# Optimization experiments

Measured on AMD Instinct MI355X. Metric: run time of the kernel, lower is better.

Reference implementation:

```python
import jax, jax.numpy as jnp
import numpy as np

K = 3   # spatial_kernel_size
M = 5   # memory_size


def setup_inputs() -> dict:
    key = jax.random.key(0)
    ks = jax.random.split(key, 16)
    C = 64
    B, H, D, W = 2, 24, 24, 24
    s = 0.05
    n = jax.random.normal
    return {
        "x": n(ks[0], (B, C, H, D, W), jnp.float32),
        "prev_memory": jnp.zeros((B, C), jnp.float32),
        "Wq": n(ks[1], (C, C), jnp.float32) * s,
        "bq": n(ks[2], (C,), jnp.float32) * s,
        "Wk": n(ks[3], (C, C), jnp.float32) * s,
        "bk": n(ks[4], (C,), jnp.float32) * s,
        "Wv": n(ks[5], (C, C), jnp.float32) * s,
        "bv": n(ks[6], (C,), jnp.float32) * s,
        "mem_key": n(ks[7], (C, M), jnp.float32),
        "mem_value": n(ks[8], (C, M), jnp.float32),
        "Wg": n(ks[9], (C, 2 * C), jnp.float32) * s,
        "bg": n(ks[10], (C,), jnp.float32) * s,
        "W_ih": n(ks[11], (3 * C, C), jnp.float32) * s,
        "W_hh": n(ks[12], (3 * C, C), jnp.float32) * s,
        "b_ih": n(ks[13], (3 * C,), jnp.float32) * s,
        "b_hh": n(ks[14], (3 * C,), jnp.float32) * s,
    }


def _patches(x, k):
    # x: (B,C,H,D,W) -> (B,C,k^3,H,D,W) local neighborhoods (zero-padded)
    B, C, H, D, W = x.shape
    p = k // 2
    xp = jnp.pad(x, ((0, 0), (0, 0), (p, p), (p, p), (p, p)))
    sl = [xp[:, :, i:i + H, j:j + D, l:l + W]
          for i in range(k) for j in range(k) for l in range(k)]
    return jnp.stack(sl, axis=2)


def reference(x, prev_memory, Wq, bq, Wk, bk, Wv, bv, mem_key, mem_value,
              Wg, bg, W_ih, W_hh, b_ih, b_hh):
    B, C, H, D, W = x.shape
    N = H * D * W
    xf = x.reshape(B, C, N)
    pf = _patches(x, K).reshape(B, C, K ** 3, N)

    # 1x1x1 conv projections (pure channel mixes)
    q = jnp.einsum('oc,bcn->bon', Wq, xf) + bq[None, :, None]            # (B,C,N)
    k_sp = jnp.einsum('oc,bcmn->bomn', Wk, pf) + bk[None, :, None, None]  # (B,C,27,N)
    v_sp = jnp.einsum('oc,bcmn->bomn', Wv, pf) + bv[None, :, None, None]

    # memory tokens broadcast over all spatial locations
    k_mem = jnp.broadcast_to(mem_key[None, :, :, None], (B, C, M, N))
    v_mem = jnp.broadcast_to(mem_value[None, :, :, None], (B, C, M, N))
    kk = jnp.concatenate([k_mem, k_sp], axis=2)   # (B,C,M+27,N)
    vv = jnp.concatenate([v_mem, v_sp], axis=2)

    # per-channel scalar attention over memory+neighborhood axis
    attn = jax.nn.softmax(q[:, :, None, :] * kk / jnp.sqrt(jnp.float32(C)), axis=2)
    out = jnp.sum(attn * vv, axis=2).reshape(B, C, H, D, W)

    # sigmoid gate over concat([x, out])
    gin = jnp.concatenate([xf, out.reshape(B, C, N)], axis=1)  # (B,2C,N)
    gate = jax.nn.sigmoid(jnp.einsum('oc,bcn->bon', Wg, gin)
                          + bg[None, :, None]).reshape(B, C, H, D, W)
    out = gate * out + (1.0 - gate) * x

    # GRU memory update on spatially pooled features (torch GRUCell math)
    mu = out.mean(axis=(2, 3, 4))                 # (B,C)
    gi = mu @ W_ih.T + b_ih
    gh = prev_memory @ W_hh.T + b_hh
    ir, iz, ii = jnp.split(gi, 3, axis=1)
    hr, hz, hn = jnp.split(gh, 3, axis=1)
    r = jax.nn.sigmoid(ir + hr)
    z = jax.nn.sigmoid(iz + hz)
    ng = jnp.tanh(ii + r * hn)
    new_memory = (1.0 - z) * ng + z * prev_memory
    return out, new_memory
```

## Files before the change

kernel.cpp:

```cpp
#include <hip/hip_runtime.h>
#include <math.h>

#define NPOS 13824
#define CDIM 64
#define BTCH 2
#define LOG2E 1.4426950408889634f
#define QSCALE (0.125f * LOG2E)

__device__ __forceinline__ unsigned int f2bf1(float f) {
  unsigned int u = __float_as_uint(f);
  return (u + 0x7FFFu + ((u >> 16) & 1u)) >> 16;
}

__global__ __launch_bounds__(256) void qkvg_kernel(
    const float* __restrict__ x,
    const float* __restrict__ Wq, const float* __restrict__ bq,
    const float* __restrict__ Wk, const float* __restrict__ bk,
    const float* __restrict__ Wv, const float* __restrict__ bv,
    const float* __restrict__ Wg,
    float* __restrict__ Qb, float* __restrict__ Kb, float* __restrict__ Vb,
    float* __restrict__ GXb, float* __restrict__ XT, float* __restrict__ pool)
{
  __shared__ __align__(16) float wqt[64*68];
  __shared__ __align__(16) float wkt[64*68];
  __shared__ __align__(16) float wvt[64*68];
  __shared__ __align__(16) float wgt[64*68];
  const int t  = threadIdx.x;
  const int bi = blockIdx.x;
  const int b  = bi / 216;
  const int n0 = (bi - b*216) * 64;
  if (bi == 0 && t < 128) pool[t] = 0.0f;

  #pragma unroll
  for (int k = 0; k < 16; ++k) {
    int idx = t + k*256;
    int lo = idx & 63, hi = idx >> 6;
    wqt[lo*68 + hi] = Wq[idx] * QSCALE;
    wkt[lo*68 + hi] = Wk[idx];
    wvt[lo*68 + hi] = Wv[idx];
    wgt[lo*68 + hi] = Wg[hi*128 + lo];
  }
  __syncthreads();

  const int c0  = (t & 15) * 4;
  const int nn0 = (t >> 4) * 4;
  const float* xbase = x + (size_t)(b*64)*NPOS + n0 + nn0;
  float aq[4][4] = {}; float ak[4][4] = {}; float av[4][4] = {}; float ag[4][4] = {};
  #pragma unroll 4
  for (int cp = 0; cp < 64; ++cp) {
    const float4 xv4 = *(const float4*)(xbase + (size_t)cp*NPOS);
    const float4 q4  = *(const float4*)&wqt[cp*68 + c0];
    const float4 k4  = *(const float4*)&wkt[cp*68 + c0];
    const float4 v4  = *(const float4*)&wvt[cp*68 + c0];
    const float4 g4  = *(const float4*)&wgt[cp*68 + c0];
    const float xa[4] = {xv4.x, xv4.y, xv4.z, xv4.w};
    const float qa[4] = {q4.x, q4.y, q4.z, q4.w};
    const float ka[4] = {k4.x, k4.y, k4.z, k4.w};
    const float va[4] = {v4.x, v4.y, v4.z, v4.w};
    const float ga[4] = {g4.x, g4.y, g4.z, g4.w};
    #pragma unroll
    for (int ci = 0; ci < 4; ++ci)
      #pragma unroll
      for (int ni = 0; ni < 4; ++ni) {
        aq[ci][ni] = fmaf(qa[ci], xa[ni], aq[ci][ni]);
        ak[ci][ni] = fmaf(ka[ci], xa[ni], ak[ci][ni]);
        av[ci][ni] = fmaf(va[ci], xa[ni], av[ci][ni]);
        ag[ci][ni] = fmaf(ga[ci], xa[ni], ag[ci][ni]);
      }
  }
  const float4 bq4 = *(const float4*)&bq[c0];
  const float4 bk4 = *(const float4*)&bk[c0];
  const float4 bv4 = *(const float4*)&bv[c0];
  #pragma unroll
  for (int ni = 0; ni < 4; ++ni) {
    const int p = b*NPOS + n0 + nn0 + ni;
    float4 o;
    o = make_float4(fmaf(bq4.x,QSCALE,aq[0][ni]), fmaf(bq4.y,QSCALE,aq[1][ni]),
                    fmaf(bq4.z,QSCALE,aq[2][ni]), fmaf(bq4.w,QSCALE,aq[3][ni]));
    *(float4*)&Qb[p*64 + c0] = o;
    o = make_float4(ak[0][ni]+bk4.x, ak[1][ni]+bk4.y, ak[2][ni]+bk4.z, ak[3][ni]+bk4.w);
    *(float4*)&Kb[p*64 + c0] = o;
    o = make_float4(av[0][ni]+bv4.x, av[1][ni]+bv4.y, av[2][ni]+bv4.z, av[3][ni]+bv4.w);
    *(float4*)&Vb[p*64 + c0] = o;
    o = make_float4(ag[0][ni], ag[1][ni], ag[2][ni], ag[3][ni]);
    *(float4*)&GXb[p*64 + c0] = o;
  }
  float4 xr[4];
  #pragma unroll
  for (int e = 0; e < 4; ++e)
    xr[e] = *(const float4*)(x + (size_t)(b*64 + c0 + e)*NPOS + n0 + nn0);
  const float xre[4][4] = {{xr[0].x,xr[0].y,xr[0].z,xr[0].w},
                           {xr[1].x,xr[1].y,xr[1].z,xr[1].w},
                           {xr[2].x,xr[2].y,xr[2].z,xr[2].w},
                           {xr[3].x,xr[3].y,xr[3].z,xr[3].w}};
  #pragma unroll
  for (int ni = 0; ni < 4; ++ni) {
    const int p = b*NPOS + n0 + nn0 + ni;
    *(float4*)&XT[p*64 + c0] = make_float4(xre[0][ni], xre[1][ni], xre[2][ni], xre[3][ni]);
  }
}

__global__ __launch_bounds__(256, 4) void attn_kernel(
    float* __restrict__ QOT,
    const float* __restrict__ Kb, const float* __restrict__ Vb,
    const float* __restrict__ GXb, const float* __restrict__ XT,
    const float* __restrict__ bk, const float* __restrict__ bv,
    const float* __restrict__ memk, const float* __restrict__ memv,
    const float* __restrict__ Wg, const float* __restrict__ bg,
    float* __restrict__ pool)
{
  __shared__ __align__(16) unsigned int kvbuf[8000];
  __shared__ __align__(16) float als[256];
  const int t = threadIdx.x;
  const int c = t & 63;
  const int w = t >> 6;

  {
    float* wgt2 = (float*)kvbuf;
    #pragma unroll
    for (int k = 0; k < 16; ++k) {
      int u = t + k*256;
      int cp = u >> 6, j = u & 63;
      wgt2[j*65 + cp] = Wg[cp*128 + 64 + j];
    }
  }
  __syncthreads();
  float wg2reg[64];
  {
    const float* wgt2 = (const float*)kvbuf;
    #pragma unroll
    for (int j = 0; j < 64; ++j) wg2reg[j] = wgt2[j*65 + c];
  }
  float mk[5], mv[5];
  #pragma unroll
  for (int m = 0; m < 5; ++m) { mk[m] = memk[c*5 + m]; mv[m] = memv[c*5 + m]; }
  const float bg_c = bg[c];
  __syncthreads();

  const int bi = blockIdx.x;
  const int b  = bi >> 9;
  const int tb = bi & 511;
  const int h0 = (tb >> 6) * 3;
  const int d0 = ((tb >> 3) & 7) * 3;
  const int w0 = (tb & 7) * 3;
  const int bN = b * NPOS;

  for (int u = t; u < 125*16; u += 256) {
    int pos = u >> 4, q4 = u & 15;
    int ph = pos / 25, pr = pos - ph*25;
    int pd = pr / 5,  pw = pr - pd*5;
    int hh = h0 - 1 + ph, dd = d0 - 1 + pd, ww = w0 - 1 + pw;
    bool inb = ((unsigned)hh < 24u) && ((unsigned)dd < 24u) && ((unsigned)ww < 24u);
    float4 kf, vf;
    if (inb) {
      const size_t off = ((size_t)(bN + hh*576 + dd*24 + ww))*64 + q4*4;
      kf = *(const float4*)(Kb + off);
      vf = *(const float4*)(Vb + off);
    } else {
      kf = ((const float4*)bk)[q4];
      vf = ((const float4*)bv)[q4];
    }
    uint4 pk;
    pk.x = (f2bf1(kf.x) << 16) | f2bf1(vf.x);
    pk.y = (f2bf1(kf.y) << 16) | f2bf1(vf.y);
    pk.z = (f2bf1(kf.z) << 16) | f2bf1(vf.z);
    pk.w = (f2bf1(kf.w) << 16) | f2bf1(vf.w);
    *(uint4*)&kvbuf[pos*64 + q4*4] = pk;
  }
  __syncthreads();

  float pacc = 0.0f;
  for (int li = w; li < 27; li += 4) {
    const int lh = li / 9, lr = li - lh*9;
    const int ld = lr / 3, lw = lr - ld*3;
    const int p  = bN + (h0+lh)*576 + (d0+ld)*24 + (w0+lw);
    const unsigned int* kvp = &kvbuf[(lh*25 + ld*5 + lw)*64 + c];

    const float q2 = QOT[p*64 + c];

    float mx0 = q2*mk[0], mx1 = q2*mk[1], mx2 = q2*mk[2], mx3 = q2*mk[3];
    mx0 = fmaxf(mx0, q2*mk[4]);
    #pragma unroll
    for (int i = 0; i < 3; ++i)
      #pragma unroll
      for (int j = 0; j < 3; ++j)
        #pragma unroll
        for (int l = 0; l < 3; ++l) {
          int s4 = i*9 + j*3 + l;
          float kf = __uint_as_float(kvp[(i*25 + j*5 + l)*64] & 0xFFFF0000u);
          float lv = q2 * kf;
          if ((s4 & 3) == 0) mx0 = fmaxf(mx0, lv);
          else if ((s4 & 3) == 1) mx1 = fmaxf(mx1, lv);
          else if ((s4 & 3) == 2) mx2 = fmaxf(mx2, lv);
          else mx3 = fmaxf(mx3, lv);
        }
    const float maxv = fmaxf(fmaxf(mx0, mx1), fmaxf(mx2, mx3));

    float s0 = 0.f, s1 = 0.f, o0 = 0.f, o1 = 0.f;
    #pragma unroll
    for (int m = 0; m < 5; ++m) {
      float pf = __builtin_amdgcn_exp2f(fmaf(q2, mk[m], -maxv));
      if (m & 1) { s1 += pf; o1 = fmaf(pf, mv[m], o1); }
      else       { s0 += pf; o0 = fmaf(pf, mv[m], o0); }
    }
    #pragma unroll
    for (int i = 0; i < 3; ++i)
      #pragma unroll
      for (int j = 0; j < 3; ++j)
        #pragma unroll
        for (int l = 0; l < 3; ++l) {
          int s4 = i*9 + j*3 + l;
          unsigned int kv = kvp[(i*25 + j*5 + l)*64];
          float kf = __uint_as_float(kv & 0xFFFF0000u);
          float vf = __uint_as_float(kv << 16);
          float pf = __builtin_amdgcn_exp2f(fmaf(q2, kf, -maxv));
          if (s4 & 1) { s1 += pf; o1 = fmaf(pf, vf, o1); }
          else        { s0 += pf; o0 = fmaf(pf, vf, o0); }
        }
    const float att = (o0 + o1) * __builtin_amdgcn_rcpf(s0 + s1);

    als[w*64 + c] = att;
    float g0 = GXb[p*64 + c] + bg_c, g1 = 0.f, g2 = 0.f, g3 = 0.f;
    #pragma unroll
    for (int j4 = 0; j4 < 16; ++j4) {
      const float4 a4 = *(const float4*)&als[w*64 + j4*4];
      g0 = fmaf(wg2reg[j4*4+0], a4.x, g0);
      g1 = fmaf(wg2reg[j4*4+1], a4.y, g1);
      g2 = fmaf(wg2reg[j4*4+2], a4.z, g2);
      g3 = fmaf(wg2reg[j4*4+3], a4.w, g3);
    }
    const float gl   = (g0 + g1) + (g2 + g3);
    const float gate = __builtin_amdgcn_rcpf(1.0f + __builtin_amdgcn_exp2f(-LOG2E * gl));
    const float xv   = XT[p*64 + c];
    const float fin  = fmaf(gate, att - xv, xv);
    QOT[p*64 + c] = fin;
    pacc += fin;
  }

  als[t] = pacc;
  __syncthreads();
  if (t < 64) {
    float s = als[t] + als[64 + t] + als[128 + t] + als[192 + t];
    atomicAdd(&pool[b*64 + t], s);
  }
}

__global__ __launch_bounds__(256) void outpool_kernel(
    const float* __restrict__ OT, float* __restrict__ out,
    const float* __restrict__ pool, const float* __restrict__ prev,
    const float* __restrict__ W_ih, const float* __restrict__ W_hh,
    const float* __restrict__ b_ih, const float* __restrict__ b_hh,
    float* __restrict__ outmem)
{
  __shared__ __align__(16) float ls[64*65];
  __shared__ __align__(16) float mu[128];
  __shared__ float gi[384];
  __shared__ float gh[384];
  const int t  = threadIdx.x;
  const int bi = blockIdx.x;
  const int b  = bi / 216;
  const int n0 = (bi - b*216) * 64;
  #pragma unroll
  for (int i = 0; i < 16; ++i) {
    int u = i*256 + t;
    int pos = u >> 6, cc = u & 63;
    ls[cc*65 + pos] = OT[(size_t)(b*NPOS + n0 + pos)*64 + cc];
  }
  if (bi == 0 && t < 128) mu[t] = pool[t] * (1.0f / (float)NPOS);
  __syncthreads();
  #pragma unroll
  for (int i = 0; i < 16; ++i) {
    int u = i*256 + t;
    int cc = u >> 6, j = u & 63;
    out[(size_t)(b*64 + cc)*NPOS + n0 + j] = ls[cc*65 + j];
  }
  if (bi != 0) return;

  {
    int r = t; if (r < 384) {
      const int b2 = r / 192, j = r - b2*192;
      const float4* wi4 = (const float4*)(W_ih + (size_t)j*64);
      const float4* wh4 = (const float4*)(W_hh + (size_t)j*64);
      const float4* mu4 = (const float4*)(mu + b2*64);
      const float4* pv4 = (const float4*)(prev + b2*64);
      float sgi = b_ih[j], sgh = b_hh[j];
      #pragma unroll
      for (int k = 0; k < 16; ++k) {
        float4 wv = wi4[k], m4 = mu4[k];
        sgi = fmaf(wv.x, m4.x, sgi); sgi = fmaf(wv.y, m4.y, sgi);
        sgi = fmaf(wv.z, m4.z, sgi); sgi = fmaf(wv.w, m4.w, sgi);
        float4 hv = wh4[k], p4 = pv4[k];
        sgh = fmaf(hv.x, p4.x, sgh); sgh = fmaf(hv.y, p4.y, sgh);
        sgh = fmaf(hv.z, p4.z, sgh); sgh = fmaf(hv.w, p4.w, sgh);
      }
      gi[r] = sgi; gh[r] = sgh;
    }
    if (t < 128) {
      const int r2 = 256 + t;
      const int b2 = r2 / 192, j = r2 - b2*192;
      const float4* wi4 = (const float4*)(W_ih + (size_t)j*64);
      const float4* wh4 = (const float4*)(W_hh + (size_t)j*64);
      const float4* mu4 = (const float4*)(mu + b2*64);
      const float4* pv4 = (const float4*)(prev + b2*64);
      float sgi = b_ih[j], sgh = b_hh[j];
      #pragma unroll
      for (int k = 0; k < 16; ++k) {
        float4 wv = wi4[k], m4 = mu4[k];
        sgi = fmaf(wv.x, m4.x, sgi); sgi = fmaf(wv.y, m4.y, sgi);
        sgi = fmaf(wv.z, m4.z, sgi); sgi = fmaf(wv.w, m4.w, sgi);
        float4 hv = wh4[k], p4 = pv4[k];
        sgh = fmaf(hv.x, p4.x, sgh); sgh = fmaf(hv.y, p4.y, sgh);
        sgh = fmaf(hv.z, p4.z, sgh); sgh = fmaf(hv.w, p4.w, sgh);
      }
      gi[r2] = sgi; gh[r2] = sgh;
    }
  }
  __syncthreads();
  if (t < 128) {
    const int b2 = t >> 6, cc = t & 63;
    float ir = gi[b2*192 + cc],       hr = gh[b2*192 + cc];
    float iz = gi[b2*192 + 64 + cc],  hz = gh[b2*192 + 64 + cc];
    float ii = gi[b2*192 + 128 + cc], hn = gh[b2*192 + 128 + cc];
    float rr = 1.0f / (1.0f + __builtin_amdgcn_exp2f(-LOG2E * (ir + hr)));
    float zz = 1.0f / (1.0f + __builtin_amdgcn_exp2f(-LOG2E * (iz + hz)));
    float ng = tanhf(ii + rr * hn);
    outmem[t] = (1.0f - zz) * ng + zz * prev[t];
  }
}

extern "C" void kernel_launch(void* const* d_in, const int* in_sizes, int n_in,
                              void* d_out, int out_size, void* d_ws, size_t ws_size,
                              hipStream_t stream) {
  const float* x    = (const float*)d_in[0];
  const float* prev = (const float*)d_in[1];
  const float* Wq   = (const float*)d_in[2];
  const float* bq   = (const float*)d_in[3];
  const float* Wk   = (const float*)d_in[4];
  const float* bk   = (const float*)d_in[5];
  const float* Wv   = (const float*)d_in[6];
  const float* bv   = (const float*)d_in[7];
  const float* memk = (const float*)d_in[8];
  const float* memv = (const float*)d_in[9];
  const float* Wg   = (const float*)d_in[10];
  const float* bg   = (const float*)d_in[11];
  const float* W_ih = (const float*)d_in[12];
  const float* W_hh = (const float*)d_in[13];
  const float* b_ih = (const float*)d_in[14];
  const float* b_hh = (const float*)d_in[15];

  float* out    = (float*)d_out;
  float* outmem = out + (size_t)BTCH*CDIM*NPOS;

  const size_t SZ = (size_t)BTCH*NPOS*CDIM;
  float* wsf  = (float*)d_ws;
  float* Qb   = wsf;
  float* Kb   = wsf + SZ;
  float* Vb   = wsf + 2*SZ;
  float* GXb  = wsf + 3*SZ;
  float* XT   = wsf + 4*SZ;
  float* pool = wsf + 5*SZ;

  qkvg_kernel<<<BTCH*216, 256, 0, stream>>>(x, Wq, bq, Wk, bk, Wv, bv, Wg,
                                            Qb, Kb, Vb, GXb, XT, pool);
  attn_kernel<<<BTCH*512, 256, 0, stream>>>(Qb, Kb, Vb, GXb, XT,
                                            bk, bv, memk, memv, Wg, bg, pool);
  outpool_kernel<<<BTCH*216, 256, 0, stream>>>(Qb, out, pool, prev,
                                               W_ih, W_hh, b_ih, b_hh, outmem);
}
```

Before: 174.1 us.

## Interleave gate-x and x buffers, pack gate weights in bf16, prefetch q, swizzle blocks

```diff
diff --git a/kernel.cpp b/kernel.cpp
--- a/kernel.cpp
+++ b/kernel.cpp
@@ -19,7 +19,7 @@
     const float* __restrict__ Wv, const float* __restrict__ bv,
     const float* __restrict__ Wg,
     float* __restrict__ Qb, float* __restrict__ Kb, float* __restrict__ Vb,
-    float* __restrict__ GXb, float* __restrict__ XT, float* __restrict__ pool)
+    float* __restrict__ GXT, float* __restrict__ pool)
 {
   __shared__ __align__(16) float wqt[64*68];
   __shared__ __align__(16) float wkt[64*68];
@@ -68,6 +68,14 @@
         ag[ci][ni] = fmaf(ga[ci], xa[ni], ag[ci][ni]);
       }
   }
+  float4 xr[4];
+  #pragma unroll
+  for (int e = 0; e < 4; ++e)
+    xr[e] = *(const float4*)(x + (size_t)(b*64 + c0 + e)*NPOS + n0 + nn0);
+  const float xre[4][4] = {{xr[0].x,xr[0].y,xr[0].z,xr[0].w},
+                           {xr[1].x,xr[1].y,xr[1].z,xr[1].w},
+                           {xr[2].x,xr[2].y,xr[2].z,xr[2].w},
+                           {xr[3].x,xr[3].y,xr[3].z,xr[3].w}};
   const float4 bq4 = *(const float4*)&bq[c0];
   const float4 bk4 = *(const float4*)&bk[c0];
   const float4 bv4 = *(const float4*)&bv[c0];
@@ -82,28 +90,17 @@
     *(float4*)&Kb[p*64 + c0] = o;
     o = make_float4(av[0][ni]+bv4.x, av[1][ni]+bv4.y, av[2][ni]+bv4.z, av[3][ni]+bv4.w);
     *(float4*)&Vb[p*64 + c0] = o;
-    o = make_float4(ag[0][ni], ag[1][ni], ag[2][ni], ag[3][ni]);
-    *(float4*)&GXb[p*64 + c0] = o;
-  }
-  float4 xr[4];
-  #pragma unroll
-  for (int e = 0; e < 4; ++e)
-    xr[e] = *(const float4*)(x + (size_t)(b*64 + c0 + e)*NPOS + n0 + nn0);
-  const float xre[4][4] = {{xr[0].x,xr[0].y,xr[0].z,xr[0].w},
-                           {xr[1].x,xr[1].y,xr[1].z,xr[1].w},
-                           {xr[2].x,xr[2].y,xr[2].z,xr[2].w},
-                           {xr[3].x,xr[3].y,xr[3].z,xr[3].w}};
-  #pragma unroll
-  for (int ni = 0; ni < 4; ++ni) {
-    const int p = b*NPOS + n0 + nn0 + ni;
-    *(float4*)&XT[p*64 + c0] = make_float4(xre[0][ni], xre[1][ni], xre[2][ni], xre[3][ni]);
+    o = make_float4(ag[0][ni], xre[0][ni], ag[1][ni], xre[1][ni]);
+    *(float4*)&GXT[(size_t)(p*64 + c0)*2]     = o;
+    o = make_float4(ag[2][ni], xre[2][ni], ag[3][ni], xre[3][ni]);
+    *(float4*)&GXT[(size_t)(p*64 + c0)*2 + 4] = o;
   }
 }
 
 __global__ __launch_bounds__(256, 4) void attn_kernel(
     float* __restrict__ QOT,
     const float* __restrict__ Kb, const float* __restrict__ Vb,
-    const float* __restrict__ GXb, const float* __restrict__ XT,
+    const float* __restrict__ GXT,
     const float* __restrict__ bk, const float* __restrict__ bv,
     const float* __restrict__ memk, const float* __restrict__ memv,
     const float* __restrict__ Wg, const float* __restrict__ bg,
@@ -125,11 +122,15 @@
     }
   }
   __syncthreads();
-  float wg2reg[64];
+  unsigned int wg2p[32];
   {
     const float* wgt2 = (const float*)kvbuf;
     #pragma unroll
-    for (int j = 0; j < 64; ++j) wg2reg[j] = wgt2[j*65 + c];
+    for (int j2 = 0; j2 < 32; ++j2) {
+      unsigned lo = f2bf1(wgt2[(2*j2)*65 + c]);
+      unsigned hi = f2bf1(wgt2[(2*j2+1)*65 + c]);
+      wg2p[j2] = lo | (hi << 16);
+    }
   }
   float mk[5], mv[5];
   #pragma unroll
@@ -137,7 +138,7 @@
   const float bg_c = bg[c];
   __syncthreads();
 
-  const int bi = blockIdx.x;
+  const int bi = (int)(blockIdx.x & 7) * 128 + (int)(blockIdx.x >> 3);
   const int b  = bi >> 9;
   const int tb = bi & 511;
   const int h0 = (tb >> 6) * 3;
@@ -170,30 +171,43 @@
   __syncthreads();
 
   float pacc = 0.0f;
-  for (int li = w; li < 27; li += 4) {
-    const int lh = li / 9, lr = li - lh*9;
-    const int ld = lr / 3, lw = lr - ld*3;
-    const int p  = bN + (h0+lh)*576 + (d0+ld)*24 + (w0+lw);
-    const unsigned int* kvp = &kvbuf[(lh*25 + ld*5 + lw)*64 + c];
-
-    const float q2 = QOT[p*64 + c];
-
-    float mx0 = q2*mk[0], mx1 = q2*mk[1], mx2 = q2*mk[2], mx3 = q2*mk[3];
-    mx0 = fmaxf(mx0, q2*mk[4]);
+  int li = w;
+  int lh = li / 9, lr = li - lh*9, ld = lr / 3, lw = lr - ld*3;
+  int p  = bN + (h0+lh)*576 + (d0+ld)*24 + (w0+lw);
+  int hb = (lh*25 + ld*5 + lw)*64 + c;
+  float q2 = QOT[p*64 + c];
+  for (; li < 27; li += 4) {
+    const int li_n = li + 4;
+    int p_n = p, hb_n = hb;
+    if (li_n < 27) {
+      const int lh2 = li_n / 9, lr2 = li_n - lh2*9;
+      const int ld2 = lr2 / 3,  lw2 = lr2 - ld2*3;
+      p_n  = bN + (h0+lh2)*576 + (d0+ld2)*24 + (w0+lw2);
+      hb_n = (lh2*25 + ld2*5 + lw2)*64 + c;
+    }
+    const float q_n = QOT[p_n*64 + c];
+    const float2 gx = *(const float2*)&GXT[(size_t)(p*64 + c)*2];
+
+    const unsigned int* kvp = &kvbuf[hb];
+    unsigned int kvreg[27];
     #pragma unroll
     for (int i = 0; i < 3; ++i)
       #pragma unroll
       for (int j = 0; j < 3; ++j)
         #pragma unroll
-        for (int l = 0; l < 3; ++l) {
-          int s4 = i*9 + j*3 + l;
-          float kf = __uint_as_float(kvp[(i*25 + j*5 + l)*64] & 0xFFFF0000u);
-          float lv = q2 * kf;
-          if ((s4 & 3) == 0) mx0 = fmaxf(mx0, lv);
-          else if ((s4 & 3) == 1) mx1 = fmaxf(mx1, lv);
-          else if ((s4 & 3) == 2) mx2 = fmaxf(mx2, lv);
-          else mx3 = fmaxf(mx3, lv);
-        }
+        for (int l = 0; l < 3; ++l)
+          kvreg[i*9 + j*3 + l] = kvp[(i*25 + j*5 + l)*64];
+    float mx0 = q2*mk[0], mx1 = q2*mk[1], mx2 = q2*mk[2], mx3 = q2*mk[3];
+    mx0 = fmaxf(mx0, q2*mk[4]);
+    #pragma unroll
+    for (int s = 0; s < 27; ++s) {
+      float kf = __uint_as_float(kvreg[s] & 0xFFFF0000u);
+      float lv = q2 * kf;
+      if ((s & 3) == 0) mx0 = fmaxf(mx0, lv);
+      else if ((s & 3) == 1) mx1 = fmaxf(mx1, lv);
+      else if ((s & 3) == 2) mx2 = fmaxf(mx2, lv);
+      else mx3 = fmaxf(mx3, lv);
+    }
     const float maxv = fmaxf(fmaxf(mx0, mx1), fmaxf(mx2, mx3));
 
     float s0 = 0.f, s1 = 0.f, o0 = 0.f, o1 = 0.f;
@@ -204,37 +218,34 @@
       else       { s0 += pf; o0 = fmaf(pf, mv[m], o0); }
     }
     #pragma unroll
-    for (int i = 0; i < 3; ++i)
-      #pragma unroll
-      for (int j = 0; j < 3; ++j)
-        #pragma unroll
-        for (int l = 0; l < 3; ++l) {
-          int s4 = i*9 + j*3 + l;
-          unsigned int kv = kvp[(i*25 + j*5 + l)*64];
-          float kf = __uint_as_float(kv & 0xFFFF0000u);
-          float vf = __uint_as_float(kv << 16);
-          float pf = __builtin_amdgcn_exp2f(fmaf(q2, kf, -maxv));
-          if (s4 & 1) { s1 += pf; o1 = fmaf(pf, vf, o1); }
-          else        { s0 += pf; o0 = fmaf(pf, vf, o0); }
-        }
+    for (int s = 0; s < 27; ++s) {
+      unsigned int kv = kvreg[s];
+      float kf = __uint_as_float(kv & 0xFFFF0000u);
+      float vf = __uint_as_float(kv << 16);
+      float pf = __builtin_amdgcn_exp2f(fmaf(q2, kf, -maxv));
+      if (s & 1) { s1 += pf; o1 = fmaf(pf, vf, o1); }
+      else       { s0 += pf; o0 = fmaf(pf, vf, o0); }
+    }
     const float att = (o0 + o1) * __builtin_amdgcn_rcpf(s0 + s1);
 
     als[w*64 + c] = att;
-    float g0 = GXb[p*64 + c] + bg_c, g1 = 0.f, g2 = 0.f, g3 = 0.f;
+    float g0 = gx.x + bg_c, g1 = 0.f, g2 = 0.f, g3 = 0.f;
     #pragma unroll
     for (int j4 = 0; j4 < 16; ++j4) {
       const float4 a4 = *(const float4*)&als[w*64 + j4*4];
-      g0 = fmaf(wg2reg[j4*4+0], a4.x, g0);
-      g1 = fmaf(wg2reg[j4*4+1], a4.y, g1);
-      g2 = fmaf(wg2reg[j4*4+2], a4.z, g2);
-      g3 = fmaf(wg2reg[j4*4+3], a4.w, g3);
+      const unsigned pk0 = wg2p[2*j4], pk1 = wg2p[2*j4+1];
+      g0 = fmaf(__uint_as_float(pk0 << 16),         a4.x, g0);
+      g1 = fmaf(__uint_as_float(pk0 & 0xFFFF0000u), a4.y, g1);
+      g2 = fmaf(__uint_as_float(pk1 << 16),         a4.z, g2);
+      g3 = fmaf(__uint_as_float(pk1 & 0xFFFF0000u), a4.w, g3);
     }
     const float gl   = (g0 + g1) + (g2 + g3);
     const float gate = __builtin_amdgcn_rcpf(1.0f + __builtin_amdgcn_exp2f(-LOG2E * gl));
-    const float xv   = XT[p*64 + c];
-    const float fin  = fmaf(gate, att - xv, xv);
+    const float fin  = fmaf(gate, att - gx.y, gx.y);
     QOT[p*64 + c] = fin;
     pacc += fin;
+
+    p = p_n; hb = hb_n; q2 = q_n;
   }
 
   als[t] = pacc;
@@ -276,44 +287,23 @@
   }
   if (bi != 0) return;
 
-  {
-    int r = t; if (r < 384) {
-      const int b2 = r / 192, j = r - b2*192;
-      const float4* wi4 = (const float4*)(W_ih + (size_t)j*64);
-      const float4* wh4 = (const float4*)(W_hh + (size_t)j*64);
-      const float4* mu4 = (const float4*)(mu + b2*64);
-      const float4* pv4 = (const float4*)(prev + b2*64);
-      float sgi = b_ih[j], sgh = b_hh[j];
-      #pragma unroll
-      for (int k = 0; k < 16; ++k) {
-        float4 wv = wi4[k], m4 = mu4[k];
-        sgi = fmaf(wv.x, m4.x, sgi); sgi = fmaf(wv.y, m4.y, sgi);
-        sgi = fmaf(wv.z, m4.z, sgi); sgi = fmaf(wv.w, m4.w, sgi);
-        float4 hv = wh4[k], p4 = pv4[k];
-        sgh = fmaf(hv.x, p4.x, sgh); sgh = fmaf(hv.y, p4.y, sgh);
-        sgh = fmaf(hv.z, p4.z, sgh); sgh = fmaf(hv.w, p4.w, sgh);
-      }
-      gi[r] = sgi; gh[r] = sgh;
-    }
-    if (t < 128) {
-      const int r2 = 256 + t;
-      const int b2 = r2 / 192, j = r2 - b2*192;
-      const float4* wi4 = (const float4*)(W_ih + (size_t)j*64);
-      const float4* wh4 = (const float4*)(W_hh + (size_t)j*64);
-      const float4* mu4 = (const float4*)(mu + b2*64);
-      const float4* pv4 = (const float4*)(prev + b2*64);
-      float sgi = b_ih[j], sgh = b_hh[j];
-      #pragma unroll
-      for (int k = 0; k < 16; ++k) {
-        float4 wv = wi4[k], m4 = mu4[k];
-        sgi = fmaf(wv.x, m4.x, sgi); sgi = fmaf(wv.y, m4.y, sgi);
-        sgi = fmaf(wv.z, m4.z, sgi); sgi = fmaf(wv.w, m4.w, sgi);
-        float4 hv = wh4[k], p4 = pv4[k];
-        sgh = fmaf(hv.x, p4.x, sgh); sgh = fmaf(hv.y, p4.y, sgh);
-        sgh = fmaf(hv.z, p4.z, sgh); sgh = fmaf(hv.w, p4.w, sgh);
-      }
-      gi[r2] = sgi; gh[r2] = sgh;
-    }
+  for (int r = t; r < 384; r += 256) {
+    const int b2 = r / 192, j = r - b2*192;
+    const float4* wi4 = (const float4*)(W_ih + (size_t)j*64);
+    const float4* wh4 = (const float4*)(W_hh + (size_t)j*64);
+    const float4* mu4 = (const float4*)(mu + b2*64);
+    const float4* pv4 = (const float4*)(prev + b2*64);
+    float sgi = b_ih[j], sgh = b_hh[j];
+    #pragma unroll
+    for (int k = 0; k < 16; ++k) {
+      float4 wv = wi4[k], m4 = mu4[k];
+      sgi = fmaf(wv.x, m4.x, sgi); sgi = fmaf(wv.y, m4.y, sgi);
+      sgi = fmaf(wv.z, m4.z, sgi); sgi = fmaf(wv.w, m4.w, sgi);
+      float4 hv = wh4[k], p4 = pv4[k];
+      sgh = fmaf(hv.x, p4.x, sgh); sgh = fmaf(hv.y, p4.y, sgh);
+      sgh = fmaf(hv.z, p4.z, sgh); sgh = fmaf(hv.w, p4.w, sgh);
+    }
+    gi[r] = sgi; gh[r] = sgh;
   }
   __syncthreads();
   if (t < 128) {
@@ -356,13 +346,12 @@
   float* Qb   = wsf;
   float* Kb   = wsf + SZ;
   float* Vb   = wsf + 2*SZ;
-  float* GXb  = wsf + 3*SZ;
-  float* XT   = wsf + 4*SZ;
+  float* GXT  = wsf + 3*SZ;
   float* pool = wsf + 5*SZ;
 
   qkvg_kernel<<<BTCH*216, 256, 0, stream>>>(x, Wq, bq, Wk, bk, Wv, bv, Wg,
-                                            Qb, Kb, Vb, GXb, XT, pool);
-  attn_kernel<<<BTCH*512, 256, 0, stream>>>(Qb, Kb, Vb, GXb, XT,
+                                            Qb, Kb, Vb, GXT, pool);
+  attn_kernel<<<BTCH*512, 256, 0, stream>>>(Qb, Kb, Vb, GXT,
                                             bk, bv, memk, memv, Wg, bg, pool);
   outpool_kernel<<<BTCH*216, 256, 0, stream>>>(Qb, out, pool, prev,
                                                W_ih, W_hh, b_ih, b_hh, outmem);
```

Measured after the change: 169.4 us. -2.7%, faster.
